# Optimization experiments

Measured on AMD Instinct MI355X. Metric: run time of the kernel, lower is better.

## Reference

```python
import jax, jax.numpy as jnp
import numpy as np

NUM_VERTS = 6890
NUM_JOINTS = 24
NUM_BETAS = 10
NUM_POSE_FEATS = 207  # 23 joints * 9
NUM_COCO_JOINTS = 19
BATCH = 1024

SMPL_PARENTS = np.array([0, 0, 0, 0, 1, 2, 3, 4, 5, 6, 7, 8, 9, 9, 9,
                         12, 13, 14, 16, 17, 18, 19, 20, 21], dtype=np.int32)


def batch_rodrigues(theta):
    """theta: [N,3] axis-angle -> [N,3,3] rotation matrices (Rodrigues)."""
    angle = jnp.linalg.norm(theta + 1e-8, axis=1, keepdims=True)  # [N,1]
    r = theta / angle                                             # [N,3]
    c = jnp.cos(angle)[:, :, None]                                # [N,1,1]
    s = jnp.sin(angle)[:, :, None]
    rx, ry, rz = r[:, 0], r[:, 1], r[:, 2]
    zeros = jnp.zeros_like(rx)
    K = jnp.stack([zeros, -rz, ry,
                   rz, zeros, -rx,
                   -ry, rx, zeros], axis=1).reshape(-1, 3, 3)     # skew(r)
    eye = jnp.eye(3, dtype=theta.dtype)
    return eye + s * K + (1.0 - c) * jnp.matmul(K, K)


def batch_global_rigid_transformation(Rs, Js, parents, rotate_base=True):
    """Rs: [B,24,3,3], Js: [B,24,3]. Returns (new_J [B,24,3], A [B,24,4,4])."""
    B = Rs.shape[0]
    dtype = Rs.dtype
    if rotate_base:
        rot_x = jnp.array([[1., 0., 0.], [0., -1., 0.], [0., 0., -1.]], dtype=dtype)
        root_rot = jnp.matmul(Rs[:, 0], rot_x)
    else:
        root_rot = Rs[:, 0]

    bottom = jnp.broadcast_to(jnp.array([0., 0., 0., 1.], dtype=dtype), (B, 1, 4))

    def make_A(R, t):  # R [B,3,3], t [B,3] -> [B,4,4]
        top = jnp.concatenate([R, t[:, :, None]], axis=2)  # [B,3,4]
        return jnp.concatenate([top, bottom], axis=1)

    results = [make_A(root_rot, Js[:, 0])]
    for i in range(1, NUM_JOINTS):
        t_rel = Js[:, i] - Js[:, parents[i]]
        A_here = make_A(Rs[:, i], t_rel)
        results.append(jnp.matmul(results[parents[i]], A_here))
    results = jnp.stack(results, axis=1)  # [B,24,4,4]

    new_J = results[:, :, :3, 3]
    # A = results - pad(results @ [J;0]) : subtract rotated rest joint from translation
    t_adj = jnp.einsum('bjpq,bjq->bjp', results[:, :, :3, :3], Js)  # [B,24,3]
    A = results.at[:, :, :3, 3].add(-t_adj)
    return new_J, A


def setup_inputs() -> dict:
    key = jax.random.key(0)
    ks = jax.random.split(key, 8)
    beta = jax.random.normal(ks[0], (BATCH, NUM_BETAS), dtype=jnp.float32)
    theta = jax.random.normal(ks[1], (BATCH, NUM_JOINTS * 3), dtype=jnp.float32) * 0.3
    v_template = jax.random.normal(ks[2], (NUM_VERTS, 3), dtype=jnp.float32)
    shapedirs = jax.random.normal(ks[3], (NUM_BETAS, NUM_VERTS * 3), dtype=jnp.float32) * 0.01
    J_regressor = jax.random.uniform(ks[4], (NUM_JOINTS, NUM_VERTS), dtype=jnp.float32) / NUM_VERTS
    posedirs = jax.random.normal(ks[5], (NUM_POSE_FEATS, NUM_VERTS * 3), dtype=jnp.float32) * 0.01
    joint_regressor = jax.random.uniform(ks[6], (NUM_COCO_JOINTS, NUM_VERTS), dtype=jnp.float32) / NUM_VERTS
    w_raw = jax.random.uniform(ks[7], (NUM_VERTS, NUM_JOINTS), dtype=jnp.float32)
    weights = w_raw / jnp.sum(w_raw, axis=1, keepdims=True)  # LBS weights, rows sum to 1
    parents = jnp.asarray(SMPL_PARENTS)
    return {"beta": beta, "theta": theta, "v_template": v_template,
            "shapedirs": shapedirs, "J_regressor": J_regressor,
            "posedirs": posedirs, "joint_regressor": joint_regressor,
            "weights": weights, "parents": parents}


def reference(beta, theta, v_template, shapedirs, J_regressor,
              posedirs, joint_regressor, weights, parents):
    B = beta.shape[0]
    parents_np = np.asarray(parents)

    # Shape blendshapes: [B,10]@[10,20670] -> [B,6890,3]
    v_shaped = jnp.matmul(beta, shapedirs).reshape(B, NUM_VERTS, 3) + v_template

    J = jnp.einsum('bvd,jv->bjd', v_shaped, J_regressor)

    # Pose rotations
    Rs = batch_rodrigues(theta.reshape(-1, 3)).reshape(B, NUM_JOINTS, 3, 3)
    pose_feature = (Rs[:, 1:] - jnp.eye(3, dtype=Rs.dtype)).reshape(B, NUM_POSE_FEATS)
    v_posed = jnp.matmul(pose_feature, posedirs).reshape(B, NUM_VERTS, 3) + v_shaped

    # Kinematic chain
    J_transformed, A = batch_global_rigid_transformation(Rs, J, parents_np, rotate_base=True)

    # Linear blend skinning: per-vertex 4x4 transforms
    T = jnp.einsum('vj,bjpq->bvpq', weights, A)  # [B,6890,4,4]
    ones = jnp.ones((B, NUM_VERTS, 1), dtype=v_posed.dtype)
    v_posed_homo = jnp.concatenate([v_posed, ones], axis=2)  # [B,6890,4]
    verts = jnp.einsum('bvpq,bvq->bvp', T[:, :, :3, :], v_posed_homo)  # [B,6890,3]

    joints = jnp.einsum('bvd,jv->bjd', verts, joint_regressor)  # [B,19,3]
    return verts, joints, Rs
```

## Files before the change

### kernel.cpp

```cpp
#include <hip/hip_runtime.h>
#include <math.h>

#define NV   6890
#define NJ   24
#define NB   10
#define NPF  207
#define NCJ  19
#define BATCHN 1024
#define NC3  (NV*3)
#define KTOT 224
#define NVP  6892

#define OUT_JOINTS_OFF (BATCHN*NV*3)
#define OUT_RS_OFF     (OUT_JOINTS_OFF + BATCHN*NCJ*3)

#define WS_JS     0
#define WS_EF     1024
#define WS_AADJT  115712
#define WS_JRB    377856
#define WS_DIRST  443392
#define WS_END    2765824

typedef __attribute__((ext_vector_type(8))) short short8;
typedef __attribute__((ext_vector_type(4))) float f32x4;

__device__ __forceinline__ unsigned short f2bf(float f) {
    unsigned u = __float_as_uint(f);
    unsigned r = u + 0x7FFFu + ((u >> 16) & 1u);
    return (unsigned short)(r >> 16);
}
__device__ __forceinline__ float bf2f(unsigned short u) {
    return __uint_as_float((unsigned)u << 16);
}

__global__ __launch_bounds__(256) void smpl_kAP(
    const float* __restrict__ pdirs, const float* __restrict__ sdirs,
    unsigned short* __restrict__ dirsT,
    const float* __restrict__ jreg, const float* __restrict__ vtmpl,
    float* __restrict__ js,
    const float* __restrict__ jointreg, unsigned short* __restrict__ jrb) {
    int bx = blockIdx.x, t = threadIdx.x;
    if (bx < 216) {
        int vt = bx;
        for (int g = t; g < 2688; g += 256) {
            int frag = g >> 6, fo = g & 63;
            int ks = frag / 6, s = frag - ks * 6;
            int l15 = fo >> 2, lg = fo & 3;
            int gc = vt * 96 + s * 16 + l15;
            int k0 = ks * 32 + lg * 8;
            unsigned short pk[8];
#pragma unroll
            for (int i = 0; i < 8; i++) {
                int k = k0 + i;
                float val = 0.f;
                if (gc < NC3) {
                    if (k < NPF) val = pdirs[(size_t)k * NC3 + gc];
                    else if (k < NPF + NB) val = sdirs[(size_t)(k - NPF) * NC3 + gc];
                }
                pk[i] = f2bf(val);
            }
            *(short8*)(dirsT + (size_t)vt * 21504 + (size_t)g * 8) = *(const short8*)pk;
        }
        return;
    }
    if (bx >= 216 + NJ) {
        int j = bx - 216 - NJ;
        for (int v = t; v < NVP; v += 256)
            jrb[(size_t)j * NVP + v] = (v < NV) ? f2bf(jointreg[(size_t)j * NV + v]) : 0;
        return;
    }
    int j = bx - 216;
    float acc[33];
#pragma unroll
    for (int e = 0; e < 33; e++) acc[e] = 0.f;
    for (int v = t; v < NV; v += 256) {
        float w = jreg[j * NV + v];
#pragma unroll
        for (int k = 0; k < NB; k++) {
#pragma unroll
            for (int d = 0; d < 3; d++)
                acc[k * 3 + d] += w * sdirs[(size_t)k * NC3 + v * 3 + d];
        }
#pragma unroll
        for (int d = 0; d < 3; d++) acc[30 + d] += w * vtmpl[v * 3 + d];
    }
#pragma unroll
    for (int e = 0; e < 33; e++) {
#pragma unroll
        for (int off = 32; off >= 1; off >>= 1) acc[e] += __shfl_xor(acc[e], off, 64);
    }
    __shared__ float red[4][33];
    int lane = t & 63, wv = t >> 6;
    if (lane == 0) {
#pragma unroll
        for (int e = 0; e < 33; e++) red[wv][e] = acc[e];
    }
    __syncthreads();
    if (t < 33) js[j * 33 + t] = red[0][t] + red[1][t] + red[2][t] + red[3][t];
}

__global__ void smpl_kB(const float* __restrict__ theta, const float* __restrict__ beta_,
                        const float* __restrict__ js, float* __restrict__ outRs,
                        unsigned short* __restrict__ ef, unsigned short* __restrict__ aadjT) {
    int b = blockIdx.x;
    int t = threadIdx.x;
    __shared__ float Rl[NJ][9];
    __shared__ float Jl[NJ][3];
    __shared__ float Rw[NJ][12];

    if (t < NJ) {
        int j = t;
        float tx = theta[b * 72 + j * 3 + 0];
        float ty = theta[b * 72 + j * 3 + 1];
        float tz = theta[b * 72 + j * 3 + 2];
        float ax = tx + 1e-8f, ay = ty + 1e-8f, az = tz + 1e-8f;
        float ang = sqrtf(ax * ax + ay * ay + az * az);
        float inv = 1.0f / ang;
        float rx = tx * inv, ry = ty * inv, rz = tz * inv;
        float s = sinf(ang), c = cosf(ang), t1 = 1.0f - c;
        float R[9];
        R[0] = 1.0f - t1 * (ry * ry + rz * rz);
        R[1] = -s * rz + t1 * rx * ry;
        R[2] =  s * ry + t1 * rx * rz;
        R[3] =  s * rz + t1 * rx * ry;
        R[4] = 1.0f - t1 * (rx * rx + rz * rz);
        R[5] = -s * rx + t1 * ry * rz;
        R[6] = -s * ry + t1 * rx * rz;
        R[7] =  s * rx + t1 * ry * rz;
        R[8] = 1.0f - t1 * (rx * rx + ry * ry);
#pragma unroll
        for (int e = 0; e < 9; e++) {
            Rl[j][e] = R[e];
            outRs[(size_t)b * 216 + j * 9 + e] = R[e];
        }
#pragma unroll
        for (int d = 0; d < 3; d++) {
            float accJ = js[j * 33 + 30 + d];
#pragma unroll
            for (int k = 0; k < NB; k++) accJ += beta_[b * NB + k] * js[j * 33 + k * 3 + d];
            Jl[j][d] = accJ;
        }
    }
    __syncthreads();
    for (int e = t; e < KTOT; e += 64) {
        float val;
        if (e < NPF) {
            int j = e / 9 + 1;
            int rc = e - (j - 1) * 9;
            val = Rl[j][rc] - ((rc == 0 || rc == 4 || rc == 8) ? 1.0f : 0.0f);
        } else if (e < NPF + NB) {
            val = beta_[b * NB + (e - NPF)];
        } else val = 0.f;
        ef[(size_t)b * KTOT + e] = f2bf(val);
    }
    if (t == 0) {
#pragma unroll
        for (int r = 0; r < 3; r++) {
            Rw[0][r * 4 + 0] =  Rl[0][r * 3 + 0];
            Rw[0][r * 4 + 1] = -Rl[0][r * 3 + 1];
            Rw[0][r * 4 + 2] = -Rl[0][r * 3 + 2];
            Rw[0][r * 4 + 3] =  Jl[0][r];
        }
        const int par[NJ] = {0,0,0,0,1,2,3,4,5,6,7,8,9,9,9,12,13,14,16,17,18,19,20,21};
#pragma unroll
        for (int i = 1; i < NJ; i++) {
            int p = par[i];
            float tr0 = Jl[i][0] - Jl[p][0];
            float tr1 = Jl[i][1] - Jl[p][1];
            float tr2 = Jl[i][2] - Jl[p][2];
#pragma unroll
            for (int r = 0; r < 3; r++) {
                float p0 = Rw[p][r * 4 + 0], p1 = Rw[p][r * 4 + 1], p2 = Rw[p][r * 4 + 2];
#pragma unroll
                for (int cc = 0; cc < 3; cc++)
                    Rw[i][r * 4 + cc] = p0 * Rl[i][0 + cc] + p1 * Rl[i][3 + cc] + p2 * Rl[i][6 + cc];
                Rw[i][r * 4 + 3] = p0 * tr0 + p1 * tr1 + p2 * tr2 + Rw[p][r * 4 + 3];
            }
        }
    }
    __syncthreads();
    for (int i = t; i < 512; i += 64) {
        int n = i >> 5, k = i & 31;
        float v = 0.f;
        if (n < 12 && k < 24) {
            int r = n >> 2, cc = n & 3;
            if (cc < 3) v = Rw[k][n];
            else v = Rw[k][r * 4 + 3] - (Rw[k][r * 4 + 0] * Jl[k][0] + Rw[k][r * 4 + 1] * Jl[k][1] +
                                         Rw[k][r * 4 + 2] * Jl[k][2]);
        }
        aadjT[(size_t)b * 512 + i] = f2bf(v);
    }
}

#define VPHI(v, bl, d) (((v) * 133 + (bl)) * 4 + (d))
__global__ __launch_bounds__(512, 4) void smpl_kC7(
    const unsigned short* __restrict__ dirsT, const float* __restrict__ vtmpl,
    const unsigned short* __restrict__ ef, const unsigned short* __restrict__ aadjT,
    const float* __restrict__ wts, float* __restrict__ outv) {
    __shared__ __align__(16) unsigned short dl[21504];
    __shared__ __align__(16) unsigned short vph[32 * 133 * 4];
    __shared__ unsigned short wbf[32][32];

    int tid = threadIdx.x;
    int vtile = blockIdx.x;
    int lane = tid & 63, wv = tid >> 6;
    int l15 = lane & 15, lg = lane >> 4;
    int fo = l15 * 4 + lg;

    {
        const uint2* src = (const uint2*)(dirsT + (size_t)vtile * 21504);
        uint2* dst = (uint2*)dl;
        for (int i = tid; i < 5376; i += 512) dst[i] = src[i];
    }
    for (int e = tid; e < 1024; e += 512) {
        int vl = e >> 5, k = e & 31;
        int gv = vtile * 32 + vl;
        float w = (k < NJ && gv < NV) ? wts[(size_t)gv * NJ + k] : 0.f;
        wbf[vl][k] = f2bf(w);
    }
    __syncthreads();

    short8 wf0 = *(const short8*)&wbf[l15][lg * 8];
    short8 wf1 = *(const short8*)&wbf[16 + l15][lg * 8];
    float vt[6];
#pragma unroll
    for (int s = 0; s < 6; s++) {
        int gcol = vtile * 96 + s * 16 + l15;
        vt[s] = (gcol < NC3) ? vtmpl[gcol] : 0.f;
    }

    for (int bt = 0; bt < 4; bt++) {
        int bb = (blockIdx.y * 4 + bt) * 128 + wv * 16;
        const short8* efr = (const short8*)(ef + (size_t)(bb + l15) * KTOT);
        short8 av[7];
#pragma unroll
        for (int ks = 0; ks < 7; ks++) av[ks] = efr[ks * 4 + lg];
        const short8* at0 = (const short8*)(aadjT + (size_t)bb * 512);
        short8 af0 = at0[fo];
        short8 af1 = at0[64 + fo];
        __builtin_amdgcn_sched_barrier(0);

        f32x4 acc[6];
#pragma unroll
        for (int s = 0; s < 6; s++) acc[s] = (f32x4){0.f, 0.f, 0.f, 0.f};
#pragma unroll
        for (int ks = 0; ks < 7; ks++) {
#pragma unroll
            for (int s = 0; s < 6; s++) {
                short8 bv = *(const short8*)&dl[((ks * 6 + s) << 9) + fo * 8];
                acc[s] = __builtin_amdgcn_mfma_f32_16x16x32_bf16(av[ks], bv, acc[s], 0, 0, 0);
            }
        }
#pragma unroll
        for (int s = 0; s < 6; s++) {
            int col = s * 16 + l15;
            int v = col / 3, d = col - v * 3;
            int bl0 = wv * 16 + lg * 4;
#pragma unroll
            for (int r = 0; r < 4; r++)
                vph[VPHI(v, bl0 + r, d)] = f2bf(acc[s][r] + vt[s]);
        }
#pragma unroll
        for (int bl2 = 0; bl2 < 16; bl2++) {
            short8 af = af0;
            af0 = af1;
            int nx = (bl2 + 2 < 16) ? (bl2 + 2) : 15;
            af1 = at0[nx * 64 + fo];
            f32x4 z = (f32x4){0.f, 0.f, 0.f, 0.f};
            f32x4 t0 = __builtin_amdgcn_mfma_f32_16x16x32_bf16(af, wf0, z, 0, 0, 0);
            f32x4 t1 = __builtin_amdgcn_mfma_f32_16x16x32_bf16(af, wf1, z, 0, 0, 0);
            int b = bb + bl2;
            int wvb = wv * 16 + bl2;
            if (lg < 3) {
                int p = lg;
                {
                    int vv = l15;
                    ushort4 xv = *(const ushort4*)&vph[VPHI(vv, wvb, 0)];
                    float o = fmaf(t0[0], bf2f(xv.x),
                              fmaf(t0[1], bf2f(xv.y), fmaf(t0[2], bf2f(xv.z), t0[3])));
                    int gv = vtile * 32 + vv;
                    if (gv < NV) outv[(size_t)b * NC3 + gv * 3 + p] = o;
                }
                {
                    int vv = 16 + l15;
                    ushort4 xv = *(const ushort4*)&vph[VPHI(vv, wvb, 0)];
                    float o = fmaf(t1[0], bf2f(xv.x),
                              fmaf(t1[1], bf2f(xv.y), fmaf(t1[2], bf2f(xv.z), t1[3])));
                    int gv = vtile * 32 + vv;
                    if (gv < NV) outv[(size_t)b * NC3 + gv * 3 + p] = o;
                }
            }
        }
    }
}

__global__ __launch_bounds__(256) void smpl_kD(
    const float* __restrict__ verts, const unsigned short* __restrict__ jrb,
    float* __restrict__ outj) {
    int tid = threadIdx.x;
    int b = blockIdx.x;
    const float* vb = verts + (size_t)b * NC3;
    float acc[57];
#pragma unroll
    for (int e = 0; e < 57; e++) acc[e] = 0.f;

    for (int it = 0; it < 7; it++) {
        int g = it * 256 + tid;
        if (g < 1723) {
            int v = g * 4;
            const float* pa = vb + v * 3;
            float2 q0 = *(const float2*)(pa + 0);
            float2 q1 = *(const float2*)(pa + 2);
            float2 q2 = *(const float2*)(pa + 4);
            float2 q3 = *(const float2*)(pa + 6);
            float2 q4 = *(const float2*)(pa + 8);
            float2 q5 = *(const float2*)(pa + 10);
#pragma unroll
            for (int j = 0; j < NCJ; j++) {
                uint2 wp = *(const uint2*)(jrb + (size_t)j * NVP + v);
                float w0 = __uint_as_float((wp.x & 0xFFFFu) << 16);
                float w1 = __uint_as_float(wp.x & 0xFFFF0000u);
                float w2 = __uint_as_float((wp.y & 0xFFFFu) << 16);
                float w3 = __uint_as_float(wp.y & 0xFFFF0000u);
                acc[j * 3 + 0] += w0 * q0.x + w1 * q1.y + w2 * q3.x + w3 * q4.y;
                acc[j * 3 + 1] += w0 * q0.y + w1 * q2.x + w2 * q3.y + w3 * q5.x;
                acc[j * 3 + 2] += w0 * q1.x + w1 * q2.y + w2 * q4.x + w3 * q5.y;
            }
        }
    }
#pragma unroll
    for (int e = 0; e < 57; e++) {
#pragma unroll
        for (int off = 32; off >= 1; off >>= 1) acc[e] += __shfl_xor(acc[e], off, 64);
    }
    __shared__ float red[4][57];
    int lane = tid & 63, wv = tid >> 6;
    if (lane == 0) {
#pragma unroll
        for (int e = 0; e < 57; e++) red[wv][e] = acc[e];
    }
    __syncthreads();
    if (tid < 57)
        outj[(size_t)b * 57 + tid] = red[0][tid] + red[1][tid] + red[2][tid] + red[3][tid];
}

extern "C" void kernel_launch(void* const* d_in, const int* in_sizes, int n_in,
                              void* d_out, int out_size, void* d_ws, size_t ws_size,
                              hipStream_t stream) {
    (void)in_sizes; (void)n_in; (void)out_size; (void)ws_size;
    const float* beta       = (const float*)d_in[0];
    const float* theta      = (const float*)d_in[1];
    const float* v_template = (const float*)d_in[2];
    const float* shapedirs  = (const float*)d_in[3];
    const float* jreg       = (const float*)d_in[4];
    const float* posedirs   = (const float*)d_in[5];
    const float* jointreg   = (const float*)d_in[6];
    const float* weights    = (const float*)d_in[7];
    float* out = (float*)d_out;
    float* ws  = (float*)d_ws;
    unsigned short* ef    = (unsigned short*)(ws + WS_EF);
    unsigned short* aadjT = (unsigned short*)(ws + WS_AADJT);
    unsigned short* jrb   = (unsigned short*)(ws + WS_JRB);
    unsigned short* dirsT = (unsigned short*)(ws + WS_DIRST);

    smpl_kAP<<<216 + NJ + NCJ, 256, 0, stream>>>(posedirs, shapedirs, dirsT,
                                                 jreg, v_template, ws + WS_JS,
                                                 jointreg, jrb);
    smpl_kB<<<BATCHN, 64, 0, stream>>>(theta, beta, ws + WS_JS, out + OUT_RS_OFF,
                                       ef, aadjT);
    dim3 gC(216, 2);
    smpl_kC7<<<gC, 512, 0, stream>>>(dirsT, v_template, ef, aadjT, weights, out);
    smpl_kD<<<BATCHN, 256, 0, stream>>>(out, jrb, out + OUT_JOINTS_OFF);
}
```

Baseline: 118.7 us.

## Restructure skinning kernel to stream vertex tiles with double-buffered async LDS loads

The main skinning kernel's grid changes from (vertex tile × batch half) to (32 column groups × 8 batch tiles). Each block now keeps its batch A-fragments in registers and loops over 6-7 vertex tiles, prefetching the next tile's blendshape directions and bf16 skinning weights into double-buffered LDS with global_load_lds. Skinning weights are pre-converted to bf16 in the prep kernel, and the direction transpose is split across six times more blocks. This targets the serialized global-to-LDS load stall before compute, at the cost of larger LDS (lower occupancy, launch bounds 512,2), fewer blocks, and an extra barrier per tile.

```diff
diff --git a/kernel.cpp b/kernel.cpp
--- a/kernel.cpp
+++ b/kernel.cpp
@@ -19,7 +19,8 @@
 #define WS_AADJT  115712
 #define WS_JRB    377856
 #define WS_DIRST  443392
-#define WS_END    2765824
+#define WS_WTB    2765824
+#define WS_END    2876416
 
 typedef __attribute__((ext_vector_type(8))) short short8;
 typedef __attribute__((ext_vector_type(4))) float f32x4;
@@ -31,6 +32,11 @@
 }
 __device__ __forceinline__ float bf2f(unsigned short u) {
     return __uint_as_float((unsigned)u << 16);
+}
+__device__ __forceinline__ void async16(unsigned short* lds, const unsigned short* g) {
+    __builtin_amdgcn_global_load_lds(
+        (const __attribute__((address_space(1))) void*)g,
+        (__attribute__((address_space(3))) void*)lds, 16, 0, 0);
 }
 
 __global__ __launch_bounds__(256) void smpl_kAP(
@@ -38,11 +44,12 @@
     unsigned short* __restrict__ dirsT,
     const float* __restrict__ jreg, const float* __restrict__ vtmpl,
     float* __restrict__ js,
-    const float* __restrict__ jointreg, unsigned short* __restrict__ jrb) {
+    const float* __restrict__ jointreg, unsigned short* __restrict__ jrb,
+    const float* __restrict__ wts, unsigned short* __restrict__ wtb) {
     int bx = blockIdx.x, t = threadIdx.x;
-    if (bx < 216) {
-        int vt = bx;
-        for (int g = t; g < 2688; g += 256) {
+    if (bx < 216 * 6) {
+        int vt = bx / 6, part = bx - (bx / 6) * 6;
+        for (int g = part * 448 + t; g < part * 448 + 448; g += 256) {
             int frag = g >> 6, fo = g & 63;
             int ks = frag / 6, s = frag - ks * 6;
             int l15 = fo >> 2, lg = fo & 3;
@@ -63,13 +70,23 @@
         }
         return;
     }
-    if (bx >= 216 + NJ) {
-        int j = bx - 216 - NJ;
+    if (bx >= 216 * 6 + NJ + NCJ) {
+        int vt = bx - (216 * 6 + NJ + NCJ);
+        for (int e = t; e < 1024; e += 256) {
+            int vl = e >> 5, k = e & 31;
+            int gv = vt * 32 + vl;
+            float w = (k < NJ && gv < NV) ? wts[(size_t)gv * NJ + k] : 0.f;
+            wtb[(size_t)vt * 1024 + e] = f2bf(w);
+        }
+        return;
+    }
+    if (bx >= 216 * 6 + NJ) {
+        int j = bx - 216 * 6 - NJ;
         for (int v = t; v < NVP; v += 256)
             jrb[(size_t)j * NVP + v] = (v < NV) ? f2bf(jointreg[(size_t)j * NV + v]) : 0;
         return;
     }
-    int j = bx - 216;
+    int j = bx - 216 * 6;
     float acc[33];
 #pragma unroll
     for (int e = 0; e < 33; e++) acc[e] = 0.f;
@@ -192,53 +209,58 @@
     }
 }
 
-#define VPHI(v, bl, d) (((v) * 133 + (bl)) * 4 + (d))
-__global__ __launch_bounds__(512, 4) void smpl_kC7(
-    const unsigned short* __restrict__ dirsT, const float* __restrict__ vtmpl,
-    const unsigned short* __restrict__ ef, const unsigned short* __restrict__ aadjT,
-    const float* __restrict__ wts, float* __restrict__ outv) {
-    __shared__ __align__(16) unsigned short dl[21504];
-    __shared__ __align__(16) unsigned short vph[32 * 133 * 4];
-    __shared__ unsigned short wbf[32][32];
+__global__ __launch_bounds__(512, 2) void smpl_kC10(
+    const unsigned short* __restrict__ dirsT, const unsigned short* __restrict__ wtb,
+    const float* __restrict__ vtmpl, const unsigned short* __restrict__ ef,
+    const unsigned short* __restrict__ aadjT, float* __restrict__ outv) {
+    __shared__ __align__(16) unsigned short Bb[2][21504];
+    __shared__ __align__(16) unsigned short Wt[2][1024];
+    __shared__ __align__(16) unsigned short vph[8][2176];
 
     int tid = threadIdx.x;
-    int vtile = blockIdx.x;
+    int cg = blockIdx.x;
+    int bt = blockIdx.y;
     int lane = tid & 63, wv = tid >> 6;
     int l15 = lane & 15, lg = lane >> 4;
     int fo = l15 * 4 + lg;
-
-    {
-        const uint2* src = (const uint2*)(dirsT + (size_t)vtile * 21504);
-        uint2* dst = (uint2*)dl;
-        for (int i = tid; i < 5376; i += 512) dst[i] = src[i];
-    }
-    for (int e = tid; e < 1024; e += 512) {
-        int vl = e >> 5, k = e & 31;
-        int gv = vtile * 32 + vl;
-        float w = (k < NJ && gv < NV) ? wts[(size_t)gv * NJ + k] : 0.f;
-        wbf[vl][k] = f2bf(w);
-    }
-    __syncthreads();
-
-    short8 wf0 = *(const short8*)&wbf[l15][lg * 8];
-    short8 wf1 = *(const short8*)&wbf[16 + l15][lg * 8];
-    float vt[6];
-#pragma unroll
-    for (int s = 0; s < 6; s++) {
-        int gcol = vtile * 96 + s * 16 + l15;
-        vt[s] = (gcol < NC3) ? vtmpl[gcol] : 0.f;
-    }
-
-    for (int bt = 0; bt < 4; bt++) {
-        int bb = (blockIdx.y * 4 + bt) * 128 + wv * 16;
-        const short8* efr = (const short8*)(ef + (size_t)(bb + l15) * KTOT);
-        short8 av[7];
-#pragma unroll
-        for (int ks = 0; ks < 7; ks++) av[ks] = efr[ks * 4 + lg];
-        const short8* at0 = (const short8*)(aadjT + (size_t)bb * 512);
-        short8 af0 = at0[fo];
-        short8 af1 = at0[64 + fo];
-        __builtin_amdgcn_sched_barrier(0);
+    int nvt = (cg < 24) ? 7 : 6;
+    int bb = bt * 128 + wv * 16;
+
+    const unsigned short* efb = ef + (size_t)(bb + l15) * KTOT;
+    short8 av[7];
+#pragma unroll
+    for (int ks = 0; ks < 7; ks++) av[ks] = *(const short8*)(efb + ks * 32 + lg * 8);
+
+    auto stage = [&](int i, int p) {
+        int vt = cg + i * 32;
+        const unsigned short* bsrc = dirsT + (size_t)vt * 21504;
+        for (int g0 = wv * 64; g0 < 2688; g0 += 512)
+            async16(&Bb[p][(size_t)g0 * 8], bsrc + ((size_t)g0 + lane) * 8);
+        if (wv < 2) {
+            int g0 = wv * 64;
+            async16(&Wt[p][g0 * 8], wtb + (size_t)vt * 1024 + ((size_t)g0 + lane) * 8);
+        }
+    };
+
+    stage(0, 0);
+    __syncthreads();
+
+    unsigned short* vp = vph[wv];
+    const short8* at0 = (const short8*)(aadjT + (size_t)bb * 512);
+
+    for (int i = 0; i < nvt; i++) {
+        int pc = i & 1;
+        if (i + 1 < nvt) stage(i + 1, pc ^ 1);
+        int vt = cg + i * 32;
+
+        short8 wf0 = *(const short8*)&Wt[pc][l15 * 32 + lg * 8];
+        short8 wf1 = *(const short8*)&Wt[pc][(16 + l15) * 32 + lg * 8];
+        float vtv[6];
+#pragma unroll
+        for (int s = 0; s < 6; s++) {
+            int gcol = vt * 96 + s * 16 + l15;
+            vtv[s] = (gcol < NC3) ? vtmpl[gcol] : 0.f;
+        }
 
         f32x4 acc[6];
 #pragma unroll
@@ -247,7 +269,7 @@
         for (int ks = 0; ks < 7; ks++) {
 #pragma unroll
             for (int s = 0; s < 6; s++) {
-                short8 bv = *(const short8*)&dl[((ks * 6 + s) << 9) + fo * 8];
+                short8 bv = *(const short8*)&Bb[pc][((ks * 6 + s) << 9) + fo * 8];
                 acc[s] = __builtin_amdgcn_mfma_f32_16x16x32_bf16(av[ks], bv, acc[s], 0, 0, 0);
             }
         }
@@ -255,11 +277,12 @@
         for (int s = 0; s < 6; s++) {
             int col = s * 16 + l15;
             int v = col / 3, d = col - v * 3;
-            int bl0 = wv * 16 + lg * 4;
 #pragma unroll
             for (int r = 0; r < 4; r++)
-                vph[VPHI(v, bl0 + r, d)] = f2bf(acc[s][r] + vt[s]);
-        }
+                vp[(v * 17 + lg * 4 + r) * 4 + d] = f2bf(acc[s][r] + vtv[s]);
+        }
+        short8 af0 = at0[fo];
+        short8 af1 = at0[64 + fo];
 #pragma unroll
         for (int bl2 = 0; bl2 < 16; bl2++) {
             short8 af = af0;
@@ -270,27 +293,27 @@
             f32x4 t0 = __builtin_amdgcn_mfma_f32_16x16x32_bf16(af, wf0, z, 0, 0, 0);
             f32x4 t1 = __builtin_amdgcn_mfma_f32_16x16x32_bf16(af, wf1, z, 0, 0, 0);
             int b = bb + bl2;
-            int wvb = wv * 16 + bl2;
             if (lg < 3) {
                 int p = lg;
                 {
                     int vv = l15;
-                    ushort4 xv = *(const ushort4*)&vph[VPHI(vv, wvb, 0)];
+                    ushort4 xv = *(const ushort4*)&vp[(vv * 17 + bl2) * 4];
                     float o = fmaf(t0[0], bf2f(xv.x),
                               fmaf(t0[1], bf2f(xv.y), fmaf(t0[2], bf2f(xv.z), t0[3])));
-                    int gv = vtile * 32 + vv;
+                    int gv = vt * 32 + vv;
                     if (gv < NV) outv[(size_t)b * NC3 + gv * 3 + p] = o;
                 }
                 {
                     int vv = 16 + l15;
-                    ushort4 xv = *(const ushort4*)&vph[VPHI(vv, wvb, 0)];
+                    ushort4 xv = *(const ushort4*)&vp[(vv * 17 + bl2) * 4];
                     float o = fmaf(t1[0], bf2f(xv.x),
                               fmaf(t1[1], bf2f(xv.y), fmaf(t1[2], bf2f(xv.z), t1[3])));
-                    int gv = vtile * 32 + vv;
+                    int gv = vt * 32 + vv;
                     if (gv < NV) outv[(size_t)b * NC3 + gv * 3 + p] = o;
                 }
             }
         }
+        __syncthreads();
     }
 }
 
@@ -362,13 +385,14 @@
     unsigned short* aadjT = (unsigned short*)(ws + WS_AADJT);
     unsigned short* jrb   = (unsigned short*)(ws + WS_JRB);
     unsigned short* dirsT = (unsigned short*)(ws + WS_DIRST);
-
-    smpl_kAP<<<216 + NJ + NCJ, 256, 0, stream>>>(posedirs, shapedirs, dirsT,
-                                                 jreg, v_template, ws + WS_JS,
-                                                 jointreg, jrb);
+    unsigned short* wtb   = (unsigned short*)(ws + WS_WTB);
+
+    smpl_kAP<<<216 * 6 + NJ + NCJ + 216, 256, 0, stream>>>(
+        posedirs, shapedirs, dirsT, jreg, v_template, ws + WS_JS,
+        jointreg, jrb, weights, wtb);
     smpl_kB<<<BATCHN, 64, 0, stream>>>(theta, beta, ws + WS_JS, out + OUT_RS_OFF,
                                        ef, aadjT);
-    dim3 gC(216, 2);
-    smpl_kC7<<<gC, 512, 0, stream>>>(dirsT, v_template, ef, aadjT, weights, out);
+    dim3 gC(32, 8);
+    smpl_kC10<<<gC, 512, 0, stream>>>(dirsT, wtb, v_template, ef, aadjT, out);
     smpl_kD<<<BATCHN, 256, 0, stream>>>(out, jrb, out + OUT_JOINTS_OFF);
 }
```

Measured after the change: 117.9 us. No clear change (-0.6%).
